# Kernel optimization log

Hardware: AMD Instinct MI355X
Metric: run time of the kernel (lower is better)

## Reference

```python
import jax, jax.numpy as jnp
import numpy as np

N_NODES = 50000
N_EDGES = 800000
IN_C = 128
HID = 64          # hidden_channels
OUT_C = 128


def _glorot(key, shape):
    fan_in, fan_out = shape[1], shape[0]
    lim = (6.0 / (fan_in + fan_out)) ** 0.5
    return jax.random.uniform(key, shape, jnp.float32, -lim, lim)


def setup_inputs() -> dict:
    key = jax.random.key(0)
    ks = jax.random.split(key, 12)
    x = jax.random.normal(ks[0], (N_NODES, IN_C), jnp.float32)
    edge_index = jax.random.randint(ks[1], (2, N_EDGES), 0, N_NODES, jnp.int64)
    # SAGEConv params: lin_l (aggregated neighbors, with bias), lin_r (self, no bias)
    # layer1: 128 -> 128 (hidden*2), layer2: 128 -> 64, layer3: 64 -> 128
    d1, d2, d3 = 2 * HID, HID, OUT_C
    return {
        "x": x,
        "edge_index": edge_index,
        "W1l": _glorot(ks[2], (d1, IN_C)), "b1": jnp.zeros((d1,), jnp.float32), "W1r": _glorot(ks[3], (d1, IN_C)),
        "W2l": _glorot(ks[4], (d2, d1)),  "b2": jnp.zeros((d2,), jnp.float32), "W2r": _glorot(ks[5], (d2, d1)),
        "W3l": _glorot(ks[6], (d3, d2)),  "b3": jnp.zeros((d3,), jnp.float32), "W3r": _glorot(ks[7], (d3, d2)),
    }


def _sage_conv(x, src, dst, Wl, bl, Wr):
    # mean-aggregate source features at destination nodes (PyG SAGEConv, aggr='mean')
    msg = x[src]                                                  # [E, d]
    agg = jax.ops.segment_sum(msg, dst, num_segments=N_NODES)     # [N, d]
    cnt = jax.ops.segment_sum(jnp.ones((src.shape[0],), x.dtype), dst, num_segments=N_NODES)
    mean = agg / jnp.maximum(cnt, 1.0)[:, None]
    return mean @ Wl.T + bl + x @ Wr.T


def reference(x, edge_index, W1l, b1, W1r, W2l, b2, W2r, W3l, b3, W3r):
    src, dst = edge_index[0], edge_index[1]
    h1 = jax.nn.relu(_sage_conv(x, src, dst, W1l, b1, W1r))   # dropout: eval mode -> identity
    h2 = jax.nn.relu(_sage_conv(h1, src, dst, W2l, b2, W2r))
    h3 = jax.nn.relu(_sage_conv(h2, src, dst, W3l, b3, W3r))
    return jnp.concatenate([h1, h2, h3], axis=1)              # torch.hstack
```

## Files before the change

### kernel.cpp

```cpp
#include <hip/hip_runtime.h>
#include <hip/hip_bf16.h>

#define N_NODES 50000
#define N_EDGES 800000

constexpr int NP = 50176;
constexpr int E4 = N_EDGES / 4;
constexpr int E8 = N_EDGES / 8;
constexpr int ATB = (E8 + 255) / 256;
constexpr int PGB = 98 * 32;
constexpr int WCB2 = (64 * 256 + 128 * 128) / 256;

typedef __attribute__((ext_vector_type(8))) short bf16x8;
typedef __attribute__((ext_vector_type(4))) float f32x4;

__device__ __forceinline__ unsigned short f2bf(float f) {
    unsigned u = __float_as_uint(f);
    u += 0x7FFFu + ((u >> 16) & 1u);
    return (unsigned short)(u >> 16);
}

__device__ __forceinline__ bf16x8 pack8(float4 f0, float4 f1) {
    bf16x8 r;
    r[0] = (short)f2bf(f0.x); r[1] = (short)f2bf(f0.y);
    r[2] = (short)f2bf(f0.z); r[3] = (short)f2bf(f0.w);
    r[4] = (short)f2bf(f1.x); r[5] = (short)f2bf(f1.y);
    r[6] = (short)f2bf(f1.z); r[7] = (short)f2bf(f1.w);
    return r;
}

__global__ void zero_kernel(int* __restrict__ p, int n) {
    int i = blockIdx.x * 256 + threadIdx.x;
    if (i < n) p[i] = 0;
}

__global__ __launch_bounds__(256, 8) void prep_kernel(
        const int* __restrict__ dst, int* __restrict__ cnt, int* __restrict__ pos,
        const float* __restrict__ x,
        const float* __restrict__ W1l, const float* __restrict__ b1,
        const float* __restrict__ W1r,
        const float* __restrict__ W2l, const float* __restrict__ W2r,
        const float* __restrict__ W3l, const float* __restrict__ W3r,
        unsigned short* __restrict__ xlb, unsigned short* __restrict__ s1b,
        unsigned short* __restrict__ Wc2, unsigned short* __restrict__ Wc3) {
    __shared__ unsigned short Asl[64 * 136];
    int b = blockIdx.x;
    int tid = threadIdx.x;
    if (b < ATB) {
        int t8 = b * 256 + tid;
        if (t8 < E8) {
            int4 d0 = reinterpret_cast<const int4*>(dst)[t8 * 2];
            int4 d1 = reinterpret_cast<const int4*>(dst)[t8 * 2 + 1];
            int4 p0, p1;
            p0.x = atomicAdd(&cnt[d0.x], 1);
            p0.y = atomicAdd(&cnt[d0.y], 1);
            p0.z = atomicAdd(&cnt[d0.z], 1);
            p0.w = atomicAdd(&cnt[d0.w], 1);
            p1.x = atomicAdd(&cnt[d1.x], 1);
            p1.y = atomicAdd(&cnt[d1.y], 1);
            p1.z = atomicAdd(&cnt[d1.z], 1);
            p1.w = atomicAdd(&cnt[d1.w], 1);
            reinterpret_cast<int4*>(pos)[t8 * 2] = p0;
            reinterpret_cast<int4*>(pos)[t8 * 2 + 1] = p1;
        }
    } else if (b < ATB + PGB) {
        int p = b - ATB;
        int ng = (p >> 5) * 8 + (p & 7);
        int cg = (p >> 3) & 3;
        if (ng >= 782) return;
        int nb0 = ng * 64;
        {
            int r = tid >> 2, q = tid & 3;
            int node = nb0 + r;
            int ncl = node < N_NODES ? node : 0;
            const float4* xp = reinterpret_cast<const float4*>(x + (size_t)ncl * 128 + q * 32);
            #pragma unroll
            for (int i = 0; i < 4; ++i) {
                float4 f0 = xp[2 * i];
                float4 f1 = xp[2 * i + 1];
                uint4 w;
                w.x = (unsigned)f2bf(f0.x) | ((unsigned)f2bf(f0.y) << 16);
                w.y = (unsigned)f2bf(f0.z) | ((unsigned)f2bf(f0.w) << 16);
                w.z = (unsigned)f2bf(f1.x) | ((unsigned)f2bf(f1.y) << 16);
                w.w = (unsigned)f2bf(f1.z) | ((unsigned)f2bf(f1.w) << 16);
                *reinterpret_cast<uint4*>(&Asl[r * 136 + q * 32 + i * 8]) = w;
            }
        }
        __syncthreads();
        int wave = tid >> 6, lane = tid & 63;
        int arow = lane & 15, kseg = lane >> 4;
        int col = cg * 64 + wave * 16 + arow;
        const float* wrow = (col < 128) ? (W1l + (size_t)col * 128)
                                        : (W1r + (size_t)(col - 128) * 128);
        bf16x8 bw[4];
        #pragma unroll
        for (int kk = 0; kk < 4; ++kk) {
            float4 f0 = *reinterpret_cast<const float4*>(wrow + kk * 32 + kseg * 8);
            float4 f1 = *reinterpret_cast<const float4*>(wrow + kk * 32 + kseg * 8 + 4);
            bw[kk] = pack8(f0, f1);
        }
        float bias_v = (col < 128) ? 0.f : b1[col - 128];
        unsigned short* outbase = (col < 128) ? xlb : s1b;
        int ocol = (col < 128) ? col : (col - 128);
        #pragma unroll
        for (int g = 0; g < 4; ++g) {
            bf16x8 a[4];
            #pragma unroll
            for (int kk = 0; kk < 4; ++kk)
                a[kk] = *reinterpret_cast<const bf16x8*>(
                    &Asl[(g * 16 + arow) * 136 + kk * 32 + kseg * 8]);
            f32x4 acc = {0.f, 0.f, 0.f, 0.f};
            #pragma unroll
            for (int kk = 0; kk < 4; ++kk)
                acc = __builtin_amdgcn_mfma_f32_16x16x32_bf16(a[kk], bw[kk], acc, 0, 0, 0);
            int gn0 = nb0 + g * 16 + kseg * 4;
            #pragma unroll
            for (int r = 0; r < 4; ++r) {
                int gn = gn0 + r;
                if (gn < N_NODES)
                    outbase[(size_t)gn * 128 + ocol] = f2bf(acc[r] + bias_v);
            }
        }
    } else {
        int idx = (b - ATB - PGB) * 256 + tid;
        if (idx < 16384) {
            int nr = idx >> 8, k = idx & 255;
            float v = (k < 128) ? W2l[nr * 128 + k] : W2r[nr * 128 + (k - 128)];
            Wc2[idx] = f2bf(v);
        } else {
            int j = idx - 16384;
            int nr = j >> 7, k = j & 127;
            float v = (k < 64) ? W3l[nr * 64 + k] : W3r[nr * 64 + (k - 64)];
            Wc3[j] = f2bf(v);
        }
    }
}

__global__ void assign_kernel(const int* __restrict__ cnt, int* __restrict__ row_ptr,
                              float* __restrict__ inv_deg, int* __restrict__ total, int n) {
    int i = blockIdx.x * blockDim.x + threadIdx.x;
    int lane = threadIdx.x & 63;
    int v = (i < n) ? cnt[i] : 0;
    int s = v;
    #pragma unroll
    for (int off = 1; off < 64; off <<= 1) {
        int t = __shfl_up(s, off);
        if (lane >= off) s += t;
    }
    int base = 0;
    if (lane == 63) base = atomicAdd(total, s);
    base = __shfl(base, 63);
    if (i < n) {
        row_ptr[i] = base + s - v;
        inv_deg[i] = 1.0f / (float)(v > 1 ? v : 1);
    }
}

__global__ void fill_kernel(const int* __restrict__ src, const int* __restrict__ dst,
                            const int* __restrict__ row_ptr,
                            const int* __restrict__ pos, int* __restrict__ edge_src) {
    int t4 = blockIdx.x * 256 + threadIdx.x;
    if (t4 < E4) {
        int4 s4 = reinterpret_cast<const int4*>(src)[t4];
        int4 d4 = reinterpret_cast<const int4*>(dst)[t4];
        int4 p4 = reinterpret_cast<const int4*>(pos)[t4];
        edge_src[row_ptr[d4.x] + p4.x] = s4.x;
        edge_src[row_ptr[d4.y] + p4.y] = s4.y;
        edge_src[row_ptr[d4.z] + p4.z] = s4.z;
        edge_src[row_ptr[d4.w] + p4.w] = s4.w;
    }
}

__global__ __launch_bounds__(256) void agg1_kernel(
        const unsigned short* __restrict__ hb,
        const int* __restrict__ row_ptr, const int* __restrict__ cnt,
        const int* __restrict__ edge_src, const float* __restrict__ inv_deg,
        const unsigned short* __restrict__ s1b,
        float* __restrict__ outF, unsigned short* __restrict__ h1b, int n) {
    constexpr int LPR = 16, EPW = 4;
    int wid = (blockIdx.x * 256 + threadIdx.x) >> 6;
    int lane = threadIdx.x & 63;
    if (wid >= n) return;
    int beg = row_ptr[wid];
    int end = beg + cnt[wid];
    float inv = inv_deg[wid];
    int sub = lane / LPR, li = lane % LPR;

    float acc[8];
    #pragma unroll
    for (int j = 0; j < 8; ++j) acc[j] = 0.f;
    for (int e0 = beg; e0 < end; e0 += 4 * EPW) {
        int ea = e0 + sub, eb = ea + EPW, ec = ea + 2 * EPW, ed = ea + 3 * EPW;
        uint4 v0 = {0u,0u,0u,0u}, v1 = {0u,0u,0u,0u}, v2 = {0u,0u,0u,0u}, v3 = {0u,0u,0u,0u};
        if (ea < end) v0 = *reinterpret_cast<const uint4*>(hb + (size_t)edge_src[ea] * 128 + li * 8);
        if (eb < end) v1 = *reinterpret_cast<const uint4*>(hb + (size_t)edge_src[eb] * 128 + li * 8);
        if (ec < end) v2 = *reinterpret_cast<const uint4*>(hb + (size_t)edge_src[ec] * 128 + li * 8);
        if (ed < end) v3 = *reinterpret_cast<const uint4*>(hb + (size_t)edge_src[ed] * 128 + li * 8);
        unsigned w;
        #define ACCW(u, j0) w = (u); acc[j0] += __uint_as_float(w << 16); acc[j0+1] += __uint_as_float(w & 0xFFFF0000u)
        ACCW(v0.x, 0); ACCW(v0.y, 2); ACCW(v0.z, 4); ACCW(v0.w, 6);
        ACCW(v1.x, 0); ACCW(v1.y, 2); ACCW(v1.z, 4); ACCW(v1.w, 6);
        ACCW(v2.x, 0); ACCW(v2.y, 2); ACCW(v2.z, 4); ACCW(v2.w, 6);
        ACCW(v3.x, 0); ACCW(v3.y, 2); ACCW(v3.z, 4); ACCW(v3.w, 6);
        #undef ACCW
    }
    #pragma unroll
    for (int off = LPR; off < 64; off <<= 1) {
        #pragma unroll
        for (int j = 0; j < 8; ++j) acc[j] += __shfl_xor(acc[j], off);
    }
    if (lane < LPR) {
        uint4 s4 = *reinterpret_cast<const uint4*>(s1b + (size_t)wid * 128 + li * 8);
        float v[8];
        v[0] = fmaxf(acc[0] * inv + __uint_as_float(s4.x << 16), 0.f);
        v[1] = fmaxf(acc[1] * inv + __uint_as_float(s4.x & 0xFFFF0000u), 0.f);
        v[2] = fmaxf(acc[2] * inv + __uint_as_float(s4.y << 16), 0.f);
        v[3] = fmaxf(acc[3] * inv + __uint_as_float(s4.y & 0xFFFF0000u), 0.f);
        v[4] = fmaxf(acc[4] * inv + __uint_as_float(s4.z << 16), 0.f);
        v[5] = fmaxf(acc[5] * inv + __uint_as_float(s4.z & 0xFFFF0000u), 0.f);
        v[6] = fmaxf(acc[6] * inv + __uint_as_float(s4.w << 16), 0.f);
        v[7] = fmaxf(acc[7] * inv + __uint_as_float(s4.w & 0xFFFF0000u), 0.f);
        float4 r0 = {v[0], v[1], v[2], v[3]};
        float4 r1 = {v[4], v[5], v[6], v[7]};
        float* op = outF + (size_t)wid * 320 + li * 8;
        *reinterpret_cast<float4*>(op) = r0;
        *reinterpret_cast<float4*>(op + 4) = r1;
        uint4 w;
        w.x = (unsigned)f2bf(v[0]) | ((unsigned)f2bf(v[1]) << 16);
        w.y = (unsigned)f2bf(v[2]) | ((unsigned)f2bf(v[3]) << 16);
        w.z = (unsigned)f2bf(v[4]) | ((unsigned)f2bf(v[5]) << 16);
        w.w = (unsigned)f2bf(v[6]) | ((unsigned)f2bf(v[7]) << 16);
        *reinterpret_cast<uint4*>(h1b + (size_t)wid * 128 + li * 8) = w;
    }
}

template<int D>
__global__ __launch_bounds__(256) void agg_kernel(
        const unsigned short* __restrict__ hb,
        const int* __restrict__ row_ptr, const int* __restrict__ cnt,
        const int* __restrict__ edge_src,
        const float* __restrict__ inv_deg, unsigned short* __restrict__ meanb, int n) {
    constexpr int LPR = D / 8;
    constexpr int EPW = 64 / LPR;
    int wid = (blockIdx.x * 256 + threadIdx.x) >> 6;
    int lane = threadIdx.x & 63;
    if (wid >= n) return;
    int beg = row_ptr[wid];
    int end = beg + cnt[wid];
    float inv = inv_deg[wid];
    int sub = lane / LPR;
    int li = lane % LPR;

    float acc[8];
    #pragma unroll
    for (int j = 0; j < 8; ++j) acc[j] = 0.f;

    for (int e0 = beg; e0 < end; e0 += 4 * EPW) {
        int ea = e0 + sub;
        int eb = ea + EPW;
        int ec = ea + 2 * EPW;
        int ed = ea + 3 * EPW;
        uint4 v0 = {0u,0u,0u,0u}, v1 = {0u,0u,0u,0u}, v2 = {0u,0u,0u,0u}, v3 = {0u,0u,0u,0u};
        if (ea < end) v0 = *reinterpret_cast<const uint4*>(hb + (size_t)edge_src[ea] * D + li * 8);
        if (eb < end) v1 = *reinterpret_cast<const uint4*>(hb + (size_t)edge_src[eb] * D + li * 8);
        if (ec < end) v2 = *reinterpret_cast<const uint4*>(hb + (size_t)edge_src[ec] * D + li * 8);
        if (ed < end) v3 = *reinterpret_cast<const uint4*>(hb + (size_t)edge_src[ed] * D + li * 8);
        unsigned w;
        #define ACCW(u, j0) w = (u); acc[j0] += __uint_as_float(w << 16); acc[j0+1] += __uint_as_float(w & 0xFFFF0000u)
        ACCW(v0.x, 0); ACCW(v0.y, 2); ACCW(v0.z, 4); ACCW(v0.w, 6);
        ACCW(v1.x, 0); ACCW(v1.y, 2); ACCW(v1.z, 4); ACCW(v1.w, 6);
        ACCW(v2.x, 0); ACCW(v2.y, 2); ACCW(v2.z, 4); ACCW(v2.w, 6);
        ACCW(v3.x, 0); ACCW(v3.y, 2); ACCW(v3.z, 4); ACCW(v3.w, 6);
        #undef ACCW
    }
    #pragma unroll
    for (int off = LPR; off < 64; off <<= 1) {
        #pragma unroll
        for (int j = 0; j < 8; ++j) acc[j] += __shfl_xor(acc[j], off);
    }
    if (lane < LPR) {
        uint4 w;
        w.x = (unsigned)f2bf(acc[0] * inv) | ((unsigned)f2bf(acc[1] * inv) << 16);
        w.y = (unsigned)f2bf(acc[2] * inv) | ((unsigned)f2bf(acc[3] * inv) << 16);
        w.z = (unsigned)f2bf(acc[4] * inv) | ((unsigned)f2bf(acc[5] * inv) << 16);
        w.w = (unsigned)f2bf(acc[6] * inv) | ((unsigned)f2bf(acc[7] * inv) << 16);
        *reinterpret_cast<uint4*>(meanb + (size_t)wid * D + li * 8) = w;
    }
}

template<int K, int DOUT, bool WB>
__global__ __launch_bounds__(256, 3) void mfma_gemm_kernel(
        const unsigned short* __restrict__ Ab,
        const unsigned short* __restrict__ Fb,
        const unsigned short* __restrict__ Wc,
        const float* __restrict__ bias,
        float* __restrict__ out, int outs,
        unsigned short* __restrict__ outb, int n) {
    constexpr int DIN = K / 2;
    constexpr int KK = K / 32;
    constexpr int NWC = DOUT / 32;
    constexpr int NWM = 4 / NWC;
    constexpr int GW = 4;
    constexpr int BM = 16 * GW * NWM;
    int wave = threadIdx.x >> 6;
    int lane = threadIdx.x & 63;
    int wc = wave % NWC;
    int wm = wave / NWC;
    int arow = lane & 15;
    int kseg = lane >> 4;

    bf16x8 b0[KK], b1[KK];
    {
        const unsigned short* wp0 = Wc + (size_t)(wc * 32 + arow) * K + kseg * 8;
        const unsigned short* wp1 = wp0 + (size_t)16 * K;
        #pragma unroll
        for (int kk = 0; kk < KK; ++kk) {
            b0[kk] = *reinterpret_cast<const bf16x8*>(wp0 + kk * 32);
            b1[kk] = *reinterpret_cast<const bf16x8*>(wp1 + kk * 32);
        }
    }
    float bv0 = bias[wc * 32 + arow];
    float bv1 = bias[wc * 32 + 16 + arow];

    int g0 = blockIdx.x * (BM / 16) + wm * GW;

    bf16x8 a0[KK], a1[KK];

    #define LOADA(g, dst)                                                          \
    {                                                                              \
        int node = (g0 + (g)) * 16 + arow;                                         \
        int ncl = node < n ? node : 0;                                             \
        _Pragma("unroll")                                                          \
        for (int kk = 0; kk < KK; ++kk) {                                          \
            int k = kk * 32 + kseg * 8;                                            \
            const unsigned short* p = (k < DIN) ? (Ab + (size_t)ncl * DIN + k)     \
                                                : (Fb + (size_t)ncl * DIN + (k - DIN)); \
            dst[kk] = *reinterpret_cast<const bf16x8*>(p);                         \
        }                                                                          \
    }

    #define COMPUTE(g, ab)                                                         \
    {                                                                              \
        f32x4 acc0 = {0.f, 0.f, 0.f, 0.f}, acc1 = {0.f, 0.f, 0.f, 0.f};           \
        _Pragma("unroll")                                                          \
        for (int kk = 0; kk < KK; ++kk) {                                          \
            acc0 = __builtin_amdgcn_mfma_f32_16x16x32_bf16(ab[kk], b0[kk], acc0, 0, 0, 0); \
            acc1 = __builtin_amdgcn_mfma_f32_16x16x32_bf16(ab[kk], b1[kk], acc1, 0, 0, 0); \
        }                                                                          \
        int gbase = (g0 + (g)) * 16 + kseg * 4;                                    \
        _Pragma("unroll")                                                          \
        for (int r = 0; r < 4; ++r) {                                              \
            int gn = gbase + r;                                                    \
            if (gn < n) {                                                          \
                int col0 = wc * 32 + arow;                                         \
                float v0 = fmaxf(acc0[r] + bv0, 0.f);                              \
                float v1 = fmaxf(acc1[r] + bv1, 0.f);                              \
                out[(size_t)gn * outs + col0] = v0;                                \
                out[(size_t)gn * outs + col0 + 16] = v1;                           \
                if constexpr (WB) {                                                \
                    outb[(size_t)gn * DOUT + col0] = f2bf(v0);                     \
                    outb[(size_t)gn * DOUT + col0 + 16] = f2bf(v1);                \
                }                                                                  \
            }                                                                      \
        }                                                                          \
    }

    LOADA(0, a0);
    #pragma unroll
    for (int gp = 0; gp < GW; gp += 2) {
        LOADA(gp + 1, a1);
        COMPUTE(gp, a0);
        if (gp + 2 < GW) LOADA(gp + 2, a0);
        COMPUTE(gp + 1, a1);
    }
    #undef LOADA
    #undef COMPUTE
}

extern "C" void kernel_launch(void* const* d_in, const int* in_sizes, int n_in,
                              void* d_out, int out_size, void* d_ws, size_t ws_size,
                              hipStream_t stream) {
    const float* x   = (const float*)d_in[0];
    const int*   ei  = (const int*)d_in[1];
    const float* W1l = (const float*)d_in[2];
    const float* b1  = (const float*)d_in[3];
    const float* W1r = (const float*)d_in[4];
    const float* W2l = (const float*)d_in[5];
    const float* b2  = (const float*)d_in[6];
    const float* W2r = (const float*)d_in[7];
    const float* W3l = (const float*)d_in[8];
    const float* b3  = (const float*)d_in[9];
    const float* W3r = (const float*)d_in[10];
    float* out = (float*)d_out;

    const int* src = ei;
    const int* dst = ei + N_EDGES;

    int* wsi = (int*)d_ws;
    int*   cnt      = wsi;
    int*   total    = wsi + NP;
    int*   row_ptr  = wsi + NP + 64;
    float* inv_deg  = (float*)(wsi + 2 * NP + 64);
    int*   edge_src = wsi + 3 * NP + 64;
    int*   pos      = edge_src + N_EDGES;
    unsigned short* Wc2 = (unsigned short*)(pos + N_EDGES);
    unsigned short* Wc3 = Wc2 + 64 * 256;
    unsigned short* meanb = Wc3 + 128 * 128;
    unsigned short* xlb = meanb + (size_t)N_NODES * 128;
    unsigned short* s1b = xlb + (size_t)N_NODES * 128;
    unsigned short* h1b = s1b + (size_t)N_NODES * 128;
    unsigned short* h2b = h1b + (size_t)N_NODES * 128;

    zero_kernel<<<(NP + 64 + 255) / 256, 256, 0, stream>>>(cnt, NP + 64);

    prep_kernel<<<ATB + PGB + WCB2, 256, 0, stream>>>(dst, cnt, pos, x,
        W1l, b1, W1r, W2l, W2r, W3l, W3r, xlb, s1b, Wc2, Wc3);

    assign_kernel<<<NP / 256, 256, 0, stream>>>(cnt, row_ptr, inv_deg, total, N_NODES);
    fill_kernel<<<(E4 + 255) / 256, 256, 0, stream>>>(src, dst, row_ptr, pos, edge_src);

    const int AGG_BLOCKS = (N_NODES + 3) / 4;
    const int GB128 = (N_NODES + 127) / 128;
    const int GB64  = (N_NODES + 63) / 64;

    agg1_kernel<<<AGG_BLOCKS, 256, 0, stream>>>(xlb, row_ptr, cnt, edge_src,
        inv_deg, s1b, out, h1b, N_NODES);

    agg_kernel<128><<<AGG_BLOCKS, 256, 0, stream>>>(h1b, row_ptr, cnt, edge_src,
        inv_deg, meanb, N_NODES);
    mfma_gemm_kernel<256, 64, true><<<GB128, 256, 0, stream>>>(meanb, h1b, Wc2, b2,
        out + 128, 320, h2b, N_NODES);

    agg_kernel<64><<<AGG_BLOCKS, 256, 0, stream>>>(h2b, row_ptr, cnt, edge_src,
        inv_deg, meanb, N_NODES);
    mfma_gemm_kernel<128, 128, false><<<GB64, 256, 0, stream>>>(meanb, h2b, Wc3, b3,
        out + 192, 320, nullptr, N_NODES);
}
```

Baseline: 219.4 us.

## Partition CSR build atomics by destination range per XCD with cursor fill

```diff
diff --git a/kernel.cpp b/kernel.cpp
--- a/kernel.cpp
+++ b/kernel.cpp
@@ -5,9 +5,11 @@
 #define N_EDGES 800000
 
 constexpr int NP = 50176;
-constexpr int E4 = N_EDGES / 4;
-constexpr int E8 = N_EDGES / 8;
-constexpr int ATB = (E8 + 255) / 256;
+constexpr int NXCD = 8;
+constexpr int NR = NP / NXCD;
+constexpr int NSTRIPE = 49;
+constexpr int ES = 16328;
+constexpr int ATB = NXCD * NSTRIPE;
 constexpr int PGB = 98 * 32;
 constexpr int WCB2 = (64 * 256 + 128 * 128) / 256;
 
@@ -35,7 +37,7 @@
 }
 
 __global__ __launch_bounds__(256, 8) void prep_kernel(
-        const int* __restrict__ dst, int* __restrict__ cnt, int* __restrict__ pos,
+        const int* __restrict__ dst, int* __restrict__ cnt,
         const float* __restrict__ x,
         const float* __restrict__ W1l, const float* __restrict__ b1,
         const float* __restrict__ W1r,
@@ -47,21 +49,20 @@
     int b = blockIdx.x;
     int tid = threadIdx.x;
     if (b < ATB) {
-        int t8 = b * 256 + tid;
-        if (t8 < E8) {
-            int4 d0 = reinterpret_cast<const int4*>(dst)[t8 * 2];
-            int4 d1 = reinterpret_cast<const int4*>(dst)[t8 * 2 + 1];
-            int4 p0, p1;
-            p0.x = atomicAdd(&cnt[d0.x], 1);
-            p0.y = atomicAdd(&cnt[d0.y], 1);
-            p0.z = atomicAdd(&cnt[d0.z], 1);
-            p0.w = atomicAdd(&cnt[d0.w], 1);
-            p1.x = atomicAdd(&cnt[d1.x], 1);
-            p1.y = atomicAdd(&cnt[d1.y], 1);
-            p1.z = atomicAdd(&cnt[d1.z], 1);
-            p1.w = atomicAdd(&cnt[d1.w], 1);
-            reinterpret_cast<int4*>(pos)[t8 * 2] = p0;
-            reinterpret_cast<int4*>(pos)[t8 * 2 + 1] = p1;
+        int xcd = b & 7, st = b >> 3;
+        int lo = xcd * NR;
+        long e0 = (long)st * ES;
+        int ne = N_EDGES - (int)e0; if (ne > ES) ne = ES;
+        if (ne > 0) {
+            int ne4 = ne >> 2;
+            const int4* dp = reinterpret_cast<const int4*>(dst + e0);
+            for (int j = tid; j < ne4; j += 256) {
+                int4 d4 = dp[j];
+                if ((unsigned)(d4.x - lo) < (unsigned)NR) atomicAdd(&cnt[d4.x], 1);
+                if ((unsigned)(d4.y - lo) < (unsigned)NR) atomicAdd(&cnt[d4.y], 1);
+                if ((unsigned)(d4.z - lo) < (unsigned)NR) atomicAdd(&cnt[d4.z], 1);
+                if ((unsigned)(d4.w - lo) < (unsigned)NR) atomicAdd(&cnt[d4.w], 1);
+            }
         }
     } else if (b < ATB + PGB) {
         int p = b - ATB;
@@ -137,6 +138,7 @@
 }
 
 __global__ void assign_kernel(const int* __restrict__ cnt, int* __restrict__ row_ptr,
+                              int* __restrict__ cursor,
                               float* __restrict__ inv_deg, int* __restrict__ total, int n) {
     int i = blockIdx.x * blockDim.x + threadIdx.x;
     int lane = threadIdx.x & 63;
@@ -151,23 +153,44 @@
     if (lane == 63) base = atomicAdd(total, s);
     base = __shfl(base, 63);
     if (i < n) {
-        row_ptr[i] = base + s - v;
+        int rp = base + s - v;
+        row_ptr[i] = rp;
+        cursor[i] = rp;
         inv_deg[i] = 1.0f / (float)(v > 1 ? v : 1);
     }
 }
 
-__global__ void fill_kernel(const int* __restrict__ src, const int* __restrict__ dst,
-                            const int* __restrict__ row_ptr,
-                            const int* __restrict__ pos, int* __restrict__ edge_src) {
-    int t4 = blockIdx.x * 256 + threadIdx.x;
-    if (t4 < E4) {
-        int4 s4 = reinterpret_cast<const int4*>(src)[t4];
-        int4 d4 = reinterpret_cast<const int4*>(dst)[t4];
-        int4 p4 = reinterpret_cast<const int4*>(pos)[t4];
-        edge_src[row_ptr[d4.x] + p4.x] = s4.x;
-        edge_src[row_ptr[d4.y] + p4.y] = s4.y;
-        edge_src[row_ptr[d4.z] + p4.z] = s4.z;
-        edge_src[row_ptr[d4.w] + p4.w] = s4.w;
+__global__ __launch_bounds__(256) void fill_kernel(
+        const int* __restrict__ src, const int* __restrict__ dst,
+        int* __restrict__ cursor, int* __restrict__ edge_src) {
+    int b = blockIdx.x;
+    int tid = threadIdx.x;
+    int xcd = b & 7, st = b >> 3;
+    int lo = xcd * NR;
+    long e0 = (long)st * ES;
+    int ne = N_EDGES - (int)e0; if (ne > ES) ne = ES;
+    if (ne <= 0) return;
+    int ne4 = ne >> 2;
+    const int4* dp = reinterpret_cast<const int4*>(dst + e0);
+    for (int j = tid; j < ne4; j += 256) {
+        int4 d4 = dp[j];
+        long i0 = e0 + 4L * j;
+        if ((unsigned)(d4.x - lo) < (unsigned)NR) {
+            int p = atomicAdd(&cursor[d4.x], 1);
+            edge_src[p] = src[i0];
+        }
+        if ((unsigned)(d4.y - lo) < (unsigned)NR) {
+            int p = atomicAdd(&cursor[d4.y], 1);
+            edge_src[p] = src[i0 + 1];
+        }
+        if ((unsigned)(d4.z - lo) < (unsigned)NR) {
+            int p = atomicAdd(&cursor[d4.z], 1);
+            edge_src[p] = src[i0 + 2];
+        }
+        if ((unsigned)(d4.w - lo) < (unsigned)NR) {
+            int p = atomicAdd(&cursor[d4.w], 1);
+            edge_src[p] = src[i0 + 3];
+        }
     }
 }
 
@@ -400,10 +423,10 @@
     int*   cnt      = wsi;
     int*   total    = wsi + NP;
     int*   row_ptr  = wsi + NP + 64;
-    float* inv_deg  = (float*)(wsi + 2 * NP + 64);
-    int*   edge_src = wsi + 3 * NP + 64;
-    int*   pos      = edge_src + N_EDGES;
-    unsigned short* Wc2 = (unsigned short*)(pos + N_EDGES);
+    int*   cursor   = wsi + 2 * NP + 64;
+    float* inv_deg  = (float*)(wsi + 3 * NP + 64);
+    int*   edge_src = wsi + 4 * NP + 64;
+    unsigned short* Wc2 = (unsigned short*)(edge_src + N_EDGES);
     unsigned short* Wc3 = Wc2 + 64 * 256;
     unsigned short* meanb = Wc3 + 128 * 128;
     unsigned short* xlb = meanb + (size_t)N_NODES * 128;
@@ -413,11 +436,11 @@
 
     zero_kernel<<<(NP + 64 + 255) / 256, 256, 0, stream>>>(cnt, NP + 64);
 
-    prep_kernel<<<ATB + PGB + WCB2, 256, 0, stream>>>(dst, cnt, pos, x,
+    prep_kernel<<<ATB + PGB + WCB2, 256, 0, stream>>>(dst, cnt, x,
         W1l, b1, W1r, W2l, W2r, W3l, W3r, xlb, s1b, Wc2, Wc3);
 
-    assign_kernel<<<NP / 256, 256, 0, stream>>>(cnt, row_ptr, inv_deg, total, N_NODES);
-    fill_kernel<<<(E4 + 255) / 256, 256, 0, stream>>>(src, dst, row_ptr, pos, edge_src);
+    assign_kernel<<<NP / 256, 256, 0, stream>>>(cnt, row_ptr, cursor, inv_deg, total, N_NODES);
+    fill_kernel<<<ATB, 256, 0, stream>>>(src, dst, cursor, edge_src);
 
     const int AGG_BLOCKS = (N_NODES + 3) / 4;
     const int GB128 = (N_NODES + 127) / 128;
```

After: 247.5 us. 1.13x slower.
